# Kernel tuning notes

Measured on AMD Instinct MI355X. Metric: run time of the kernel, lower is better.

Reference implementation:

```python
import jax, jax.numpy as jnp
import numpy as np

N = 50000  # nodes
E = 800000  # edges (avg degree 16)


def gcn_agg(x, senders, receivers, n, add_self_edges):
    """jraph.GraphConvolution aggregation with symmetric normalization.
    x: [n, d] node feats already passed through update_node_fn."""
    if add_self_edges:
        idx = jnp.arange(n, dtype=senders.dtype)
        s = jnp.concatenate([senders, idx])
        r = jnp.concatenate([receivers, idx])
    else:
        s, r = senders, receivers
    ones = jnp.ones(s.shape, x.dtype)
    sdeg = jax.ops.segment_sum(ones, s, num_segments=n)
    rdeg = jax.ops.segment_sum(ones, r, num_segments=n)
    x = x * jax.lax.rsqrt(jnp.maximum(sdeg, 1.0))[:, None]
    x = jax.ops.segment_sum(x[s], r, num_segments=n)  # [E+,d] gather -> scatter-sum
    return x * jax.lax.rsqrt(jnp.maximum(rdeg, 1.0))[:, None]


def setup_inputs() -> dict:
    key = jax.random.key(0)
    ks = jax.random.split(key, 9)
    d_in, d_h, d_z, d_out = 128, 128, 64, 128

    def w(k, i, o):
        return jax.random.normal(k, (i, o), jnp.float32) / np.float32(np.sqrt(i))

    return {
        "nodes": jax.random.normal(ks[0], (N, d_in), jnp.float32),
        "senders": jax.random.randint(ks[1], (E,), 0, N, jnp.int32),
        "receivers": jax.random.randint(ks[2], (E,), 0, N, jnp.int32),
        "eps": jax.random.normal(ks[3], (N, d_z), jnp.float32),
        "W_h": w(ks[4], d_in, d_h), "b_h": jnp.zeros((d_h,), jnp.float32),
        "W_mu": w(ks[5], d_h, d_z), "b_mu": jnp.zeros((d_z,), jnp.float32),
        "W_ls": w(ks[6], d_h, d_z), "b_ls": jnp.zeros((d_z,), jnp.float32),
        "W_dh": w(ks[7], d_z, d_h), "b_dh": jnp.zeros((d_h,), jnp.float32),
        "W_do": w(ks[8], d_h, d_out), "b_do": jnp.zeros((d_out,), jnp.float32),
    }


def reference(nodes, senders, receivers, eps, W_h, b_h, W_mu, b_mu,
              W_ls, b_ls, W_dh, b_dh, W_do, b_do):
    n = nodes.shape[0]
    # encoder hidden GCN (add_self_edges=True): Linear+elu update, then agg.
    # (the first of the two identical encoder GCN calls in the source is dead
    #  code -- both read the original graph, only the 2nd result is used)
    h = jax.nn.elu(nodes @ W_h + b_h)
    h = gcn_agg(h, senders, receivers, n, True)
    # mean / log_std GCNs (add_self_edges=False)
    mean = gcn_agg(h @ W_mu + b_mu, senders, receivers, n, False)
    log_std = gcn_agg(h @ W_ls + b_ls, senders, receivers, n, False)
    # reparameterization
    z = mean + jnp.exp(log_std) * eps
    # decoder: GCN(self edges, Linear+elu) -> GCN(no self edges, Linear)
    d = jax.nn.elu(z @ W_dh + b_dh)
    d = gcn_agg(d, senders, receivers, n, True)
    out = gcn_agg(d @ W_do + b_do, senders, receivers, n, False)
    return mean, log_std, out
```

## Files before the change

kernel.cpp:

```cpp
#include <hip/hip_runtime.h>
#include <hip/hip_bf16.h>
#include <hip/hip_fp16.h>
#include <math.h>


typedef _Float16 f16x8 __attribute__((ext_vector_type(8)));
typedef _Float16 f16x4 __attribute__((ext_vector_type(4)));
typedef float    f32x4 __attribute__((ext_vector_type(4)));

union H2x4 { int4 i; __half2 h[4]; };

#define HSL 64
#define HIST_LDS_W 12544
#define NSLICE 256
#define CAP 8000

__global__ __launch_bounds__(256)
void hist8s_k(const int* __restrict__ snd, unsigned int* __restrict__ partial,
              int nE, int nW)
{
    __shared__ unsigned int sh[HIST_LDS_W];
    const int slice = blockIdx.x;
    for (int w = threadIdx.x; w < nW; w += 256) sh[w] = 0u;
    __syncthreads();
    const int per = (nE + HSL - 1) / HSL;
    const int e1 = min(nE, slice * per + per);
    for (int e = slice * per + threadIdx.x; e < e1; e += 256) {
        int v = snd[e];
        atomicAdd(&sh[v >> 2], 1u << ((v & 3) * 8));
    }
    __syncthreads();
    unsigned int* dst = partial + (size_t)slice * nW;
    for (int w = threadIdx.x; w < nW; w += 256) dst[w] = sh[w];
}

__global__ __launch_bounds__(256)
void hist8s_reduce_k(const unsigned int* __restrict__ partial,
                     float* __restrict__ dsi, float* __restrict__ dsn,
                     int n, int nW)
{
    int w = blockIdx.x * 256 + threadIdx.x;
    if (w >= nW) return;
    const unsigned int* src = partial + w;
    int c0 = 0, c1 = 0, c2 = 0, c3 = 0;
    for (int s = 0; s < HSL; ++s) {
        unsigned int v = src[(size_t)s * nW];
        c0 += v & 255u; c1 += (v >> 8) & 255u; c2 += (v >> 16) & 255u; c3 += v >> 24;
    }
    const int cc[4] = {c0, c1, c2, c3};
    const int node0 = w * 4;
#pragma unroll
    for (int u = 0; u < 4; ++u) {
        int node = node0 + u;
        if (node >= n) break;
        float fd = (float)cc[u];
        dsi[node] = rsqrtf(fd + 1.0f);
        dsn[node] = rsqrtf(fmaxf(fd, 1.0f));
    }
}

__global__ __launch_bounds__(256)
void rcount_k(const int* __restrict__ rcv, int* __restrict__ cnt, int nE, int nb)
{
    __shared__ int lc[256];
    const int s = blockIdx.x;
    if (threadIdx.x < nb) lc[threadIdx.x] = 0;
    __syncthreads();
    const int per = (nE + NSLICE - 1) / NSLICE;
    const int e1 = min(nE, (s + 1) * per);
    for (int e = s * per + threadIdx.x; e < e1; e += 256)
        atomicAdd(&lc[rcv[e] >> 8], 1);
    __syncthreads();
    if (threadIdx.x < nb) cnt[s * nb + threadIdx.x] = lc[threadIdx.x];
}

__global__ __launch_bounds__(256)
void rscan_k(const int* __restrict__ cnt, int* __restrict__ sbase,
             int* __restrict__ btot, int nb)
{
    __shared__ int sh[256];
    const int b = blockIdx.x, t = threadIdx.x;
    int v = cnt[t * nb + b];
    sh[t] = v; __syncthreads();
#pragma unroll
    for (int off = 1; off < 256; off <<= 1) {
        int u = (t >= off) ? sh[t - off] : 0;
        __syncthreads(); sh[t] += u; __syncthreads();
    }
    sbase[t * nb + b] = sh[t] - v;
    if (t == 255) btot[b] = sh[255];
}

__global__ __launch_bounds__(256)
void bscan_k(const int* __restrict__ btot, int* __restrict__ bbase,
             int* __restrict__ row_start, int nb, int n)
{
    __shared__ int sh[256];
    const int t = threadIdx.x;
    int v = (t < nb) ? btot[t] : 0;
    sh[t] = v; __syncthreads();
#pragma unroll
    for (int off = 1; off < 256; off <<= 1) {
        int u = (t >= off) ? sh[t - off] : 0;
        __syncthreads(); sh[t] += u; __syncthreads();
    }
    if (t < nb) bbase[t] = sh[t] - v;
    if (t == 255) row_start[n] = sh[255];
}

__global__ __launch_bounds__(256)
void rscatter_k(const int* __restrict__ snd, const int* __restrict__ rcv,
                const int* __restrict__ sbase, int2* __restrict__ stage,
                int nE, int nb)
{
    __shared__ int cur[256];
    const int s = blockIdx.x;
    if (threadIdx.x < nb) cur[threadIdx.x] = sbase[s * nb + threadIdx.x];
    __syncthreads();
    const int per = (nE + NSLICE - 1) / NSLICE;
    const int e1 = min(nE, (s + 1) * per);
    for (int e = s * per + threadIdx.x; e < e1; e += 256) {
        int r = rcv[e], b = r >> 8;
        int t = atomicAdd(&cur[b], 1);
        if (t < CAP) stage[(size_t)b * CAP + t] = make_int2(snd[e], r);
    }
}

__global__ __launch_bounds__(256)
void rfin_k(const int2* __restrict__ stage, const int* __restrict__ btot,
            const int* __restrict__ bbase, int* __restrict__ row_start,
            float* __restrict__ dri, float* __restrict__ drn,
            int* __restrict__ csr, int n)
{
    __shared__ int cnt[256];
    __shared__ int pos[256];
    __shared__ int lbuf[CAP];
    const int b = blockIdx.x, t = threadIdx.x;
    cnt[t] = 0;
    __syncthreads();
    const int tot = min(btot[b], CAP);
    const int2* sp = stage + (size_t)b * CAP;
    for (int i = t; i < tot; i += 256)
        atomicAdd(&cnt[sp[i].y & 255], 1);
    __syncthreads();
    const int c = cnt[t];
    pos[t] = c; __syncthreads();
#pragma unroll
    for (int off = 1; off < 256; off <<= 1) {
        int u = (t >= off) ? pos[t - off] : 0;
        __syncthreads(); pos[t] += u; __syncthreads();
    }
    const int excl = pos[t] - c;
    const int base = bbase[b];
    const int v = b * 256 + t;
    if (v < n) {
        row_start[v] = base + excl;
        float fd = (float)c;
        dri[v] = rsqrtf(fd + 1.0f);
        drn[v] = rsqrtf(fmaxf(fd, 1.0f));
    }
    cnt[t] = excl;
    __syncthreads();
    for (int i = t; i < tot; i += 256) {
        int2 p = sp[i];
        int q = atomicAdd(&cnt[p.y & 255], 1);
        lbuf[q] = p.x << 8;
    }
    __syncthreads();
    for (int i = t; i < tot; i += 256)
        csr[base + i] = lbuf[i];
}

__global__ __launch_bounds__(256)
void wprep_k(const float* __restrict__ W_h, const float* __restrict__ W_mu,
             const float* __restrict__ W_ls, const float* __restrict__ W_dh,
             const float* __restrict__ W_do,
             const float* __restrict__ b_mu, const float* __restrict__ b_ls,
             __half* __restrict__ WT_h, __half* __restrict__ WT2,
             __half* __restrict__ WT_dh, __half* __restrict__ WT_do,
             float* __restrict__ bias2)
{
    int gid = blockIdx.x * 256 + threadIdx.x;
    if (gid < 16384) {
        int m = gid >> 7, k = gid & 127;
        WT_h[gid] = __float2half(W_h[k * 128 + m]);
    } else if (gid < 32768) {
        int t = gid - 16384; int m = t >> 7, k = t & 127;
        float v = (m < 64) ? W_mu[k * 64 + m] : W_ls[k * 64 + (m - 64)];
        WT2[t] = __float2half(v);
    } else if (gid < 40960) {
        int t = gid - 32768; int m = t >> 6, k = t & 63;
        WT_dh[t] = __float2half(W_dh[k * 128 + m]);
    } else if (gid < 57344) {
        int t = gid - 40960; int m = t >> 7, k = t & 127;
        WT_do[t] = __float2half(W_do[k * 128 + m]);
    } else if (gid < 57472) {
        int c = gid - 57344;
        bias2[c] = (c < 64) ? b_mu[c] : b_ls[c - 64];
    }
}

template<int K, int ELU, typename XT>
__global__ __launch_bounds__(256)
void mgemm_k(const XT* __restrict__ X, const __half* __restrict__ WT,
             const float* __restrict__ Bias, const float* __restrict__ rowscale,
             __half* __restrict__ Y, int nrows)
{
    const int lane = threadIdx.x & 63;
    const int w    = threadIdx.x >> 6;
    const int l15  = lane & 15, l4 = lane >> 4;
    const int rowbase = blockIdx.x * 128 + w * 32;
    if (rowbase >= nrows) return;

    f32x4 acc[2][8];
#pragma unroll
    for (int mt = 0; mt < 2; ++mt)
#pragma unroll
        for (int nt = 0; nt < 8; ++nt)
#pragma unroll
            for (int q = 0; q < 4; ++q) acc[mt][nt][q] = 0.f;

    const int r0 = min(rowbase + l15,      nrows - 1);
    const int r1 = min(rowbase + 16 + l15, nrows - 1);

#pragma unroll
    for (int ks = 0; ks < K / 32; ++ks) {
        const int ko = ks * 32 + l4 * 8;
        f16x8 a0, a1;
        if constexpr (sizeof(XT) == 4) {
            const float4 p0 = *(const float4*)&X[(size_t)r0 * K + ko];
            const float4 p1 = *(const float4*)&X[(size_t)r0 * K + ko + 4];
            const float4 q0 = *(const float4*)&X[(size_t)r1 * K + ko];
            const float4 q1 = *(const float4*)&X[(size_t)r1 * K + ko + 4];
            a0[0] = (_Float16)p0.x; a0[1] = (_Float16)p0.y;
            a0[2] = (_Float16)p0.z; a0[3] = (_Float16)p0.w;
            a0[4] = (_Float16)p1.x; a0[5] = (_Float16)p1.y;
            a0[6] = (_Float16)p1.z; a0[7] = (_Float16)p1.w;
            a1[0] = (_Float16)q0.x; a1[1] = (_Float16)q0.y;
            a1[2] = (_Float16)q0.z; a1[3] = (_Float16)q0.w;
            a1[4] = (_Float16)q1.x; a1[5] = (_Float16)q1.y;
            a1[6] = (_Float16)q1.z; a1[7] = (_Float16)q1.w;
        } else {
            a0 = *(const f16x8*)&X[(size_t)r0 * K + ko];
            a1 = *(const f16x8*)&X[(size_t)r1 * K + ko];
        }
#pragma unroll
        for (int nt = 0; nt < 8; ++nt) {
            const f16x8 b = *(const f16x8*)&WT[(size_t)(nt * 16 + l15) * K + ko];
            acc[0][nt] = __builtin_amdgcn_mfma_f32_16x16x32_f16(b, a0, acc[0][nt], 0, 0, 0);
            acc[1][nt] = __builtin_amdgcn_mfma_f32_16x16x32_f16(b, a1, acc[1][nt], 0, 0, 0);
        }
    }

    const int xr0 = rowbase + l15, xr1 = rowbase + 16 + l15;
    const float rs0 = (xr0 < nrows) ? rowscale[xr0] : 0.f;
    const float rs1 = (xr1 < nrows) ? rowscale[xr1] : 0.f;
#pragma unroll
    for (int nt = 0; nt < 8; ++nt) {
        const float4 b4 = *(const float4*)&Bias[nt * 16 + l4 * 4];
        const float bb[4] = {b4.x, b4.y, b4.z, b4.w};
        f16x4 o0, o1;
#pragma unroll
        for (int i = 0; i < 4; ++i) {
            float v0 = acc[0][nt][i] + bb[i];
            float v1 = acc[1][nt][i] + bb[i];
            if (ELU) {
                v0 = (v0 > 0.f) ? v0 : expm1f(v0);
                v1 = (v1 > 0.f) ? v1 : expm1f(v1);
            }
            o0[i] = (_Float16)(v0 * rs0);
            o1[i] = (_Float16)(v1 * rs1);
        }
        if (xr0 < nrows) *(f16x4*)&Y[(size_t)xr0 * 128 + nt * 16 + l4 * 4] = o0;
        if (xr1 < nrows) *(f16x4*)&Y[(size_t)xr1 * 128 + nt * 16 + l4 * 4] = o1;
    }
}

__device__ inline void agg_core(const char* __restrict__ yb, const int* __restrict__ csr,
                                int beg, int end, int g, float2 (&acc)[4])
{
    int j = beg;
    if (j + 16 <= end) {
        int o0 = csr[j + g], o1 = csr[j + 4 + g];
        int o2 = csr[j + 8 + g], o3 = csr[j + 12 + g];
        for (; j + 32 <= end; j += 16) {
            const int p0 = csr[j + 16 + g], p1 = csr[j + 20 + g];
            const int p2 = csr[j + 24 + g], p3 = csr[j + 28 + g];
            H2x4 r0, r1, r2, r3;
            r0.i = *(const int4*)(yb + o0);
            r1.i = *(const int4*)(yb + o1);
            r2.i = *(const int4*)(yb + o2);
            r3.i = *(const int4*)(yb + o3);
#pragma unroll
            for (int k = 0; k < 4; ++k) {
                const float2 f01 = __half22float2(__hadd2(r0.h[k], r1.h[k]));
                const float2 f23 = __half22float2(__hadd2(r2.h[k], r3.h[k]));
                acc[k].x += f01.x + f23.x;
                acc[k].y += f01.y + f23.y;
            }
            o0 = p0; o1 = p1; o2 = p2; o3 = p3;
        }
        {
            H2x4 r0, r1, r2, r3;
            r0.i = *(const int4*)(yb + o0);
            r1.i = *(const int4*)(yb + o1);
            r2.i = *(const int4*)(yb + o2);
            r3.i = *(const int4*)(yb + o3);
#pragma unroll
            for (int k = 0; k < 4; ++k) {
                const float2 f01 = __half22float2(__hadd2(r0.h[k], r1.h[k]));
                const float2 f23 = __half22float2(__hadd2(r2.h[k], r3.h[k]));
                acc[k].x += f01.x + f23.x;
                acc[k].y += f01.y + f23.y;
            }
        }
        j += 16;
    }
    for (; j + 8 <= end; j += 8) {
        const int o0 = csr[j + g], o1 = csr[j + 4 + g];
        H2x4 r0, r1;
        r0.i = *(const int4*)(yb + o0);
        r1.i = *(const int4*)(yb + o1);
#pragma unroll
        for (int k = 0; k < 4; ++k) {
            const float2 f01 = __half22float2(__hadd2(r0.h[k], r1.h[k]));
            acc[k].x += f01.x;
            acc[k].y += f01.y;
        }
    }
    for (; j < end; j += 4) {
        const int e = j + g;
        const bool ok = e < end;
        const int o = csr[ok ? e : end - 1];
        H2x4 r; r.i = *(const int4*)(yb + o);
        if (ok) {
#pragma unroll
            for (int k = 0; k < 4; ++k) {
                const float2 f = __half22float2(r.h[k]);
                acc[k].x += f.x;
                acc[k].y += f.y;
            }
        }
    }
#pragma unroll
    for (int k = 0; k < 4; ++k) {
        acc[k].x += __shfl_xor(acc[k].x, 16);
        acc[k].y += __shfl_xor(acc[k].y, 16);
        acc[k].x += __shfl_xor(acc[k].x, 32);
        acc[k].y += __shfl_xor(acc[k].y, 32);
    }
}

__global__ __launch_bounds__(256)
void aggw_self_k(const __half* __restrict__ y, const int* __restrict__ row_start,
                 const int* __restrict__ csr, const float* __restrict__ rsc,
                 __half* __restrict__ out, int n)
{
    const int v    = (blockIdx.x * 256 + threadIdx.x) >> 6;
    const int lane = threadIdx.x & 63;
    if (v >= n) return;
    const int g = lane >> 4, c16 = lane & 15;
    const int beg = row_start[v], end = row_start[v + 1];
    const char* yb = (const char*)y + c16 * 16;

    float2 acc[4] = {{0.f,0.f},{0.f,0.f},{0.f,0.f},{0.f,0.f}};
    if (g == 0) {
        H2x4 r; r.i = *(const int4*)(yb + (v << 8));
#pragma unroll
        for (int k = 0; k < 4; ++k) {
            const float2 f = __half22float2(r.h[k]);
            acc[k].x += f.x; acc[k].y += f.y;
        }
    }
    agg_core(yb, csr, beg, end, g, acc);
    if (g == 0) {
        const float sc = rsc[v];
        f16x8 o;
#pragma unroll
        for (int k = 0; k < 4; ++k) {
            o[2 * k]     = (_Float16)(acc[k].x * sc);
            o[2 * k + 1] = (_Float16)(acc[k].y * sc);
        }
        *(f16x8*)&out[(size_t)v * 128 + c16 * 8] = o;
    }
}

__global__ __launch_bounds__(256)
void aggw_f32_k(const __half* __restrict__ y, const int* __restrict__ row_start,
                const int* __restrict__ csr, const float* __restrict__ rsc,
                float* __restrict__ out, int n)
{
    const int v    = (blockIdx.x * 256 + threadIdx.x) >> 6;
    const int lane = threadIdx.x & 63;
    if (v >= n) return;
    const int g = lane >> 4, c16 = lane & 15;
    const int beg = row_start[v], end = row_start[v + 1];
    const char* yb = (const char*)y + c16 * 16;

    float2 acc[4] = {{0.f,0.f},{0.f,0.f},{0.f,0.f},{0.f,0.f}};
    agg_core(yb, csr, beg, end, g, acc);
    const float sc = rsc[v];
    if (g == 0)
        *(float4*)&out[(size_t)v * 128 + c16 * 8] =
            make_float4(acc[0].x * sc, acc[0].y * sc, acc[1].x * sc, acc[1].y * sc);
    if (g == 1)
        *(float4*)&out[(size_t)v * 128 + c16 * 8 + 4] =
            make_float4(acc[2].x * sc, acc[2].y * sc, acc[3].x * sc, acc[3].y * sc);
}

__global__ __launch_bounds__(256)
void aggw_2z_k(const __half* __restrict__ y, const int* __restrict__ row_start,
               const int* __restrict__ csr, const float* __restrict__ rsc,
               const float* __restrict__ eps,
               float* __restrict__ mean, float* __restrict__ lstd,
               __half* __restrict__ z16, int n)
{
    const int v    = (blockIdx.x * 256 + threadIdx.x) >> 6;
    const int lane = threadIdx.x & 63;
    if (v >= n) return;
    const int g = lane >> 4, c16 = lane & 15;
    const int beg = row_start[v], end = row_start[v + 1];
    const char* yb = (const char*)y + c16 * 16;

    float2 acc2[4] = {{0.f,0.f},{0.f,0.f},{0.f,0.f},{0.f,0.f}};
    agg_core(yb, csr, beg, end, g, acc2);
    const float sc = rsc[v];
    float acc[8];
#pragma unroll
    for (int k = 0; k < 4; ++k) {
        acc[2 * k]     = acc2[k].x * sc;
        acc[2 * k + 1] = acc2[k].y * sc;
    }

    if (c16 < 8) {
        if (g == 0) *(float4*)&mean[(size_t)v * 64 + c16 * 8]     = make_float4(acc[0], acc[1], acc[2], acc[3]);
        if (g == 1) *(float4*)&mean[(size_t)v * 64 + c16 * 8 + 4] = make_float4(acc[4], acc[5], acc[6], acc[7]);
    } else {
        if (g == 0) *(float4*)&lstd[(size_t)v * 64 + (c16 - 8) * 8]     = make_float4(acc[0], acc[1], acc[2], acc[3]);
        if (g == 1) *(float4*)&lstd[(size_t)v * 64 + (c16 - 8) * 8 + 4] = make_float4(acc[4], acc[5], acc[6], acc[7]);
    }
    float lsv[8];
#pragma unroll
    for (int k = 0; k < 8; ++k) lsv[k] = __shfl_xor(acc[k], 8);
    if (g == 0 && c16 < 8) {
        const float4 e0 = *(const float4*)&eps[(size_t)v * 64 + c16 * 8];
        const float4 e1 = *(const float4*)&eps[(size_t)v * 64 + c16 * 8 + 4];
        const float ev[8] = {e0.x, e0.y, e0.z, e0.w, e1.x, e1.y, e1.z, e1.w};
        f16x8 o;
#pragma unroll
        for (int k = 0; k < 8; ++k) o[k] = (_Float16)(acc[k] + expf(lsv[k]) * ev[k]);
        *(f16x8*)&z16[(size_t)v * 64 + c16 * 8] = o;
    }
}

extern "C" void kernel_launch(void* const* d_in, const int* in_sizes, int n_in,
                              void* d_out, int out_size, void* d_ws, size_t ws_size,
                              hipStream_t stream)
{
    const float* nodes = (const float*)d_in[0];
    const int*   snd   = (const int*)d_in[1];
    const int*   rcv   = (const int*)d_in[2];
    const float* eps   = (const float*)d_in[3];
    const float* W_h  = (const float*)d_in[4];  const float* b_h  = (const float*)d_in[5];
    const float* W_mu = (const float*)d_in[6];  const float* b_mu = (const float*)d_in[7];
    const float* W_ls = (const float*)d_in[8];  const float* b_ls = (const float*)d_in[9];
    const float* W_dh = (const float*)d_in[10]; const float* b_dh = (const float*)d_in[11];
    const float* W_do = (const float*)d_in[12]; const float* b_do = (const float*)d_in[13];

    const int n  = in_sizes[0] / 128;
    const int nE = in_sizes[1];
    const int nW = (n + 3) >> 2;
    const int nb = (n + 255) >> 8;

    __half* bufA16 = (__half*)d_ws;
    __half* bufB16 = bufA16 + (size_t)n * 128;
    __half* bufC16 = bufB16 + (size_t)n * 128;
    float* dsi = (float*)(bufC16 + (size_t)n * 64);
    float* dri = dsi + n;
    float* dsn = dri + n;
    float* drn = dsn + n;
    int* row_start = (int*)(drn + n);
    int* csr       = row_start + n + 4;
    int* cnt       = csr + nE;
    int* sbase     = cnt + 256 * nb;
    int* btot      = sbase + 256 * nb;
    int* bbase     = btot + 256;
    __half* WT_h  = (__half*)(bbase + 256);
    __half* WT2   = WT_h + 16384;
    __half* WT_dh = WT2 + 16384;
    __half* WT_do = WT_dh + 8192;
    float*  bias2 = (float*)(WT_do + 16384);
    unsigned int* partial = (unsigned int*)bufA16;
    int2* stage = (int2*)bufB16;

    float* mean = (float*)d_out;
    float* lstd = mean + (size_t)n * 64;
    float* outp = lstd + (size_t)n * 64;

    auto cdiv = [](int a, int b) { return (a + b - 1) / b; };
    const int gG = cdiv(n, 128);
    const int gW = cdiv(n * 64, 256);

    wprep_k<<<cdiv(57472, 256), 256, 0, stream>>>(W_h, W_mu, W_ls, W_dh, W_do,
                                                  b_mu, b_ls, WT_h, WT2, WT_dh, WT_do, bias2);
    hist8s_k<<<HSL, 256, 0, stream>>>(snd, partial, nE, nW);
    hist8s_reduce_k<<<cdiv(nW, 256), 256, 0, stream>>>(partial, dsi, dsn, n, nW);
    rcount_k<<<NSLICE, 256, 0, stream>>>(rcv, cnt, nE, nb);
    rscan_k<<<nb, 256, 0, stream>>>(cnt, sbase, btot, nb);
    bscan_k<<<1, 256, 0, stream>>>(btot, bbase, row_start, nb, n);
    rscatter_k<<<NSLICE, 256, 0, stream>>>(snd, rcv, sbase, stage, nE, nb);
    rfin_k<<<nb, 256, 0, stream>>>(stage, btot, bbase, row_start, dri, drn, csr, n);

    mgemm_k<128, 1, float><<<gG, 256, 0, stream>>>(nodes, WT_h, b_h, dsi, bufA16, n);
    aggw_self_k<<<gW, 256, 0, stream>>>(bufA16, row_start, csr, dri, bufB16, n);

    mgemm_k<128, 0, __half><<<gG, 256, 0, stream>>>(bufB16, WT2, bias2, dsn, bufA16, n);
    aggw_2z_k<<<gW, 256, 0, stream>>>(bufA16, row_start, csr, drn, eps, mean, lstd, bufC16, n);

    mgemm_k<64, 1, __half><<<gG, 256, 0, stream>>>(bufC16, WT_dh, b_dh, dsi, bufA16, n);
    aggw_self_k<<<gW, 256, 0, stream>>>(bufA16, row_start, csr, dri, bufB16, n);

    mgemm_k<128, 0, __half><<<gG, 256, 0, stream>>>(bufB16, WT_do, b_do, dsn, bufA16, n);
    aggw_f32_k<<<gW, 256, 0, stream>>>(bufA16, row_start, csr, drn, outp, n);
}
```

Before: 275.3 us.

## Map one node per 16-lane group in aggregation and merge CSR count/scatter

The aggregation kernels now assign one node to each 16-lane quarter of a wavefront, so a wave handles four nodes. Each lane walks that node's full edge list serially, replacing the old scheme where four groups split the edges of one node and combined them with cross-lane shuffles. The CSR build drops its separate count, per-slice scan and scatter kernels for one kernel that reserves bucket ranges with global atomics. This cuts launches and shuffle reductions, but per-node load imbalance grows and edges land in buckets in a nondeterministic order.

Result: no change. 270.6 us (median of 2 runs) (-1.7%).

```diff
diff --git a/kernel.cpp b/kernel.cpp
--- a/kernel.cpp
+++ b/kernel.cpp
@@ -60,35 +60,29 @@
 }
 
 __global__ __launch_bounds__(256)
-void rcount_k(const int* __restrict__ rcv, int* __restrict__ cnt, int nE, int nb)
+void rscatter2_k(const int* __restrict__ snd, const int* __restrict__ rcv,
+                 int* __restrict__ gcur, int2* __restrict__ stage,
+                 int nE, int nb)
 {
     __shared__ int lc[256];
-    const int s = blockIdx.x;
-    if (threadIdx.x < nb) lc[threadIdx.x] = 0;
+    __shared__ int lbase[256];
+    const int s = blockIdx.x, t = threadIdx.x;
+    lc[t] = 0;
     __syncthreads();
     const int per = (nE + NSLICE - 1) / NSLICE;
-    const int e1 = min(nE, (s + 1) * per);
-    for (int e = s * per + threadIdx.x; e < e1; e += 256)
+    const int e0 = s * per, e1 = min(nE, e0 + per);
+    for (int e = e0 + t; e < e1; e += 256)
         atomicAdd(&lc[rcv[e] >> 8], 1);
     __syncthreads();
-    if (threadIdx.x < nb) cnt[s * nb + threadIdx.x] = lc[threadIdx.x];
-}
-
-__global__ __launch_bounds__(256)
-void rscan_k(const int* __restrict__ cnt, int* __restrict__ sbase,
-             int* __restrict__ btot, int nb)
-{
-    __shared__ int sh[256];
-    const int b = blockIdx.x, t = threadIdx.x;
-    int v = cnt[t * nb + b];
-    sh[t] = v; __syncthreads();
-#pragma unroll
-    for (int off = 1; off < 256; off <<= 1) {
-        int u = (t >= off) ? sh[t - off] : 0;
-        __syncthreads(); sh[t] += u; __syncthreads();
-    }
-    sbase[t * nb + b] = sh[t] - v;
-    if (t == 255) btot[b] = sh[255];
+    if (t < nb && lc[t] > 0) lbase[t] = atomicAdd(&gcur[t], lc[t]);
+    __syncthreads();
+    lc[t] = 0;
+    __syncthreads();
+    for (int e = e0 + t; e < e1; e += 256) {
+        int r = rcv[e], b = r >> 8;
+        int q = lbase[b] + atomicAdd(&lc[b], 1);
+        if (q < CAP) stage[(size_t)b * CAP + q] = make_int2(snd[e], r);
+    }
 }
 
 __global__ __launch_bounds__(256)
@@ -106,24 +100,6 @@
     }
     if (t < nb) bbase[t] = sh[t] - v;
     if (t == 255) row_start[n] = sh[255];
-}
-
-__global__ __launch_bounds__(256)
-void rscatter_k(const int* __restrict__ snd, const int* __restrict__ rcv,
-                const int* __restrict__ sbase, int2* __restrict__ stage,
-                int nE, int nb)
-{
-    __shared__ int cur[256];
-    const int s = blockIdx.x;
-    if (threadIdx.x < nb) cur[threadIdx.x] = sbase[s * nb + threadIdx.x];
-    __syncthreads();
-    const int per = (nE + NSLICE - 1) / NSLICE;
-    const int e1 = min(nE, (s + 1) * per);
-    for (int e = s * per + threadIdx.x; e < e1; e += 256) {
-        int r = rcv[e], b = r >> 8;
-        int t = atomicAdd(&cur[b], 1);
-        if (t < CAP) stage[(size_t)b * CAP + t] = make_int2(snd[e], r);
-    }
 }
 
 __global__ __launch_bounds__(256)
@@ -276,154 +252,106 @@
     }
 }
 
-__device__ inline void agg_core(const char* __restrict__ yb, const int* __restrict__ csr,
-                                int beg, int end, int g, float2 (&acc)[4])
+__device__ inline void agg_core2(const char* __restrict__ yb, const int* __restrict__ csr,
+                                 int beg, int end, float2 (&acc)[4])
 {
     int j = beg;
-    if (j + 16 <= end) {
-        int o0 = csr[j + g], o1 = csr[j + 4 + g];
-        int o2 = csr[j + 8 + g], o3 = csr[j + 12 + g];
-        for (; j + 32 <= end; j += 16) {
-            const int p0 = csr[j + 16 + g], p1 = csr[j + 20 + g];
-            const int p2 = csr[j + 24 + g], p3 = csr[j + 28 + g];
-            H2x4 r0, r1, r2, r3;
-            r0.i = *(const int4*)(yb + o0);
-            r1.i = *(const int4*)(yb + o1);
-            r2.i = *(const int4*)(yb + o2);
-            r3.i = *(const int4*)(yb + o3);
-#pragma unroll
-            for (int k = 0; k < 4; ++k) {
-                const float2 f01 = __half22float2(__hadd2(r0.h[k], r1.h[k]));
-                const float2 f23 = __half22float2(__hadd2(r2.h[k], r3.h[k]));
-                acc[k].x += f01.x + f23.x;
-                acc[k].y += f01.y + f23.y;
-            }
-            o0 = p0; o1 = p1; o2 = p2; o3 = p3;
-        }
-        {
-            H2x4 r0, r1, r2, r3;
-            r0.i = *(const int4*)(yb + o0);
-            r1.i = *(const int4*)(yb + o1);
-            r2.i = *(const int4*)(yb + o2);
-            r3.i = *(const int4*)(yb + o3);
-#pragma unroll
-            for (int k = 0; k < 4; ++k) {
-                const float2 f01 = __half22float2(__hadd2(r0.h[k], r1.h[k]));
-                const float2 f23 = __half22float2(__hadd2(r2.h[k], r3.h[k]));
-                acc[k].x += f01.x + f23.x;
-                acc[k].y += f01.y + f23.y;
-            }
-        }
-        j += 16;
-    }
-    for (; j + 8 <= end; j += 8) {
-        const int o0 = csr[j + g], o1 = csr[j + 4 + g];
-        H2x4 r0, r1;
+    for (; j + 4 <= end; j += 4) {
+        const int o0 = csr[j], o1 = csr[j + 1], o2 = csr[j + 2], o3 = csr[j + 3];
+        H2x4 r0, r1, r2, r3;
         r0.i = *(const int4*)(yb + o0);
         r1.i = *(const int4*)(yb + o1);
+        r2.i = *(const int4*)(yb + o2);
+        r3.i = *(const int4*)(yb + o3);
 #pragma unroll
         for (int k = 0; k < 4; ++k) {
             const float2 f01 = __half22float2(__hadd2(r0.h[k], r1.h[k]));
-            acc[k].x += f01.x;
-            acc[k].y += f01.y;
+            const float2 f23 = __half22float2(__hadd2(r2.h[k], r3.h[k]));
+            acc[k].x += f01.x + f23.x;
+            acc[k].y += f01.y + f23.y;
         }
     }
-    for (; j < end; j += 4) {
-        const int e = j + g;
-        const bool ok = e < end;
-        const int o = csr[ok ? e : end - 1];
+    for (; j < end; ++j) {
+        const int o = csr[j];
         H2x4 r; r.i = *(const int4*)(yb + o);
-        if (ok) {
-#pragma unroll
-            for (int k = 0; k < 4; ++k) {
-                const float2 f = __half22float2(r.h[k]);
-                acc[k].x += f.x;
-                acc[k].y += f.y;
-            }
+#pragma unroll
+        for (int k = 0; k < 4; ++k) {
+            const float2 f = __half22float2(r.h[k]);
+            acc[k].x += f.x;
+            acc[k].y += f.y;
         }
     }
-#pragma unroll
-    for (int k = 0; k < 4; ++k) {
-        acc[k].x += __shfl_xor(acc[k].x, 16);
-        acc[k].y += __shfl_xor(acc[k].y, 16);
-        acc[k].x += __shfl_xor(acc[k].x, 32);
-        acc[k].y += __shfl_xor(acc[k].y, 32);
-    }
-}
-
-__global__ __launch_bounds__(256)
-void aggw_self_k(const __half* __restrict__ y, const int* __restrict__ row_start,
+}
+
+__global__ __launch_bounds__(256)
+void aggg_self_k(const __half* __restrict__ y, const int* __restrict__ row_start,
                  const int* __restrict__ csr, const float* __restrict__ rsc,
                  __half* __restrict__ out, int n)
 {
-    const int v    = (blockIdx.x * 256 + threadIdx.x) >> 6;
-    const int lane = threadIdx.x & 63;
+    const int wid = (blockIdx.x * 256 + threadIdx.x) >> 6;
+    const int g   = (threadIdx.x >> 4) & 3;
+    const int l16 = threadIdx.x & 15;
+    const int v   = wid * 4 + g;
     if (v >= n) return;
-    const int g = lane >> 4, c16 = lane & 15;
     const int beg = row_start[v], end = row_start[v + 1];
-    const char* yb = (const char*)y + c16 * 16;
-
-    float2 acc[4] = {{0.f,0.f},{0.f,0.f},{0.f,0.f},{0.f,0.f}};
-    if (g == 0) {
+    const char* yb = (const char*)y + l16 * 16;
+
+    float2 acc[4];
+    {
         H2x4 r; r.i = *(const int4*)(yb + (v << 8));
 #pragma unroll
-        for (int k = 0; k < 4; ++k) {
-            const float2 f = __half22float2(r.h[k]);
-            acc[k].x += f.x; acc[k].y += f.y;
-        }
-    }
-    agg_core(yb, csr, beg, end, g, acc);
-    if (g == 0) {
-        const float sc = rsc[v];
-        f16x8 o;
-#pragma unroll
-        for (int k = 0; k < 4; ++k) {
-            o[2 * k]     = (_Float16)(acc[k].x * sc);
-            o[2 * k + 1] = (_Float16)(acc[k].y * sc);
-        }
-        *(f16x8*)&out[(size_t)v * 128 + c16 * 8] = o;
-    }
-}
-
-__global__ __launch_bounds__(256)
-void aggw_f32_k(const __half* __restrict__ y, const int* __restrict__ row_start,
+        for (int k = 0; k < 4; ++k) acc[k] = __half22float2(r.h[k]);
+    }
+    agg_core2(yb, csr, beg, end, acc);
+    const float sc = rsc[v];
+    f16x8 o;
+#pragma unroll
+    for (int k = 0; k < 4; ++k) {
+        o[2 * k]     = (_Float16)(acc[k].x * sc);
+        o[2 * k + 1] = (_Float16)(acc[k].y * sc);
+    }
+    *(f16x8*)&out[(size_t)v * 128 + l16 * 8] = o;
+}
+
+__global__ __launch_bounds__(256)
+void aggg_f32_k(const __half* __restrict__ y, const int* __restrict__ row_start,
                 const int* __restrict__ csr, const float* __restrict__ rsc,
                 float* __restrict__ out, int n)
 {
-    const int v    = (blockIdx.x * 256 + threadIdx.x) >> 6;
-    const int lane = threadIdx.x & 63;
+    const int wid = (blockIdx.x * 256 + threadIdx.x) >> 6;
+    const int g   = (threadIdx.x >> 4) & 3;
+    const int l16 = threadIdx.x & 15;
+    const int v   = wid * 4 + g;
     if (v >= n) return;
-    const int g = lane >> 4, c16 = lane & 15;
     const int beg = row_start[v], end = row_start[v + 1];
-    const char* yb = (const char*)y + c16 * 16;
+    const char* yb = (const char*)y + l16 * 16;
 
     float2 acc[4] = {{0.f,0.f},{0.f,0.f},{0.f,0.f},{0.f,0.f}};
-    agg_core(yb, csr, beg, end, g, acc);
+    agg_core2(yb, csr, beg, end, acc);
     const float sc = rsc[v];
-    if (g == 0)
-        *(float4*)&out[(size_t)v * 128 + c16 * 8] =
-            make_float4(acc[0].x * sc, acc[0].y * sc, acc[1].x * sc, acc[1].y * sc);
-    if (g == 1)
-        *(float4*)&out[(size_t)v * 128 + c16 * 8 + 4] =
-            make_float4(acc[2].x * sc, acc[2].y * sc, acc[3].x * sc, acc[3].y * sc);
-}
-
-__global__ __launch_bounds__(256)
-void aggw_2z_k(const __half* __restrict__ y, const int* __restrict__ row_start,
+    *(float4*)&out[(size_t)v * 128 + l16 * 8] =
+        make_float4(acc[0].x * sc, acc[0].y * sc, acc[1].x * sc, acc[1].y * sc);
+    *(float4*)&out[(size_t)v * 128 + l16 * 8 + 4] =
+        make_float4(acc[2].x * sc, acc[2].y * sc, acc[3].x * sc, acc[3].y * sc);
+}
+
+__global__ __launch_bounds__(256)
+void aggg_2z_k(const __half* __restrict__ y, const int* __restrict__ row_start,
                const int* __restrict__ csr, const float* __restrict__ rsc,
                const float* __restrict__ eps,
                float* __restrict__ mean, float* __restrict__ lstd,
                __half* __restrict__ z16, int n)
 {
-    const int v    = (blockIdx.x * 256 + threadIdx.x) >> 6;
-    const int lane = threadIdx.x & 63;
+    const int wid = (blockIdx.x * 256 + threadIdx.x) >> 6;
+    const int g   = (threadIdx.x >> 4) & 3;
+    const int l16 = threadIdx.x & 15;
+    const int v   = wid * 4 + g;
     if (v >= n) return;
-    const int g = lane >> 4, c16 = lane & 15;
     const int beg = row_start[v], end = row_start[v + 1];
-    const char* yb = (const char*)y + c16 * 16;
+    const char* yb = (const char*)y + l16 * 16;
 
     float2 acc2[4] = {{0.f,0.f},{0.f,0.f},{0.f,0.f},{0.f,0.f}};
-    agg_core(yb, csr, beg, end, g, acc2);
+    agg_core2(yb, csr, beg, end, acc2);
     const float sc = rsc[v];
     float acc[8];
 #pragma unroll
@@ -432,24 +360,24 @@
         acc[2 * k + 1] = acc2[k].y * sc;
     }
 
-    if (c16 < 8) {
-        if (g == 0) *(float4*)&mean[(size_t)v * 64 + c16 * 8]     = make_float4(acc[0], acc[1], acc[2], acc[3]);
-        if (g == 1) *(float4*)&mean[(size_t)v * 64 + c16 * 8 + 4] = make_float4(acc[4], acc[5], acc[6], acc[7]);
+    if (l16 < 8) {
+        *(float4*)&mean[(size_t)v * 64 + l16 * 8]     = make_float4(acc[0], acc[1], acc[2], acc[3]);
+        *(float4*)&mean[(size_t)v * 64 + l16 * 8 + 4] = make_float4(acc[4], acc[5], acc[6], acc[7]);
     } else {
-        if (g == 0) *(float4*)&lstd[(size_t)v * 64 + (c16 - 8) * 8]     = make_float4(acc[0], acc[1], acc[2], acc[3]);
-        if (g == 1) *(float4*)&lstd[(size_t)v * 64 + (c16 - 8) * 8 + 4] = make_float4(acc[4], acc[5], acc[6], acc[7]);
+        *(float4*)&lstd[(size_t)v * 64 + (l16 - 8) * 8]     = make_float4(acc[0], acc[1], acc[2], acc[3]);
+        *(float4*)&lstd[(size_t)v * 64 + (l16 - 8) * 8 + 4] = make_float4(acc[4], acc[5], acc[6], acc[7]);
     }
     float lsv[8];
 #pragma unroll
     for (int k = 0; k < 8; ++k) lsv[k] = __shfl_xor(acc[k], 8);
-    if (g == 0 && c16 < 8) {
-        const float4 e0 = *(const float4*)&eps[(size_t)v * 64 + c16 * 8];
-        const float4 e1 = *(const float4*)&eps[(size_t)v * 64 + c16 * 8 + 4];
+    if (l16 < 8) {
+        const float4 e0 = *(const float4*)&eps[(size_t)v * 64 + l16 * 8];
+        const float4 e1 = *(const float4*)&eps[(size_t)v * 64 + l16 * 8 + 4];
         const float ev[8] = {e0.x, e0.y, e0.z, e0.w, e1.x, e1.y, e1.z, e1.w};
         f16x8 o;
 #pragma unroll
         for (int k = 0; k < 8; ++k) o[k] = (_Float16)(acc[k] + expf(lsv[k]) * ev[k]);
-        *(f16x8*)&z16[(size_t)v * 64 + c16 * 8] = o;
+        *(f16x8*)&z16[(size_t)v * 64 + l16 * 8] = o;
     }
 }
 
@@ -481,10 +409,8 @@
     float* drn = dsn + n;
     int* row_start = (int*)(drn + n);
     int* csr       = row_start + n + 4;
-    int* cnt       = csr + nE;
-    int* sbase     = cnt + 256 * nb;
-    int* btot      = sbase + 256 * nb;
-    int* bbase     = btot + 256;
+    int* gcur      = csr + nE;
+    int* bbase     = gcur + 256;
     __half* WT_h  = (__half*)(bbase + 256);
     __half* WT2   = WT_h + 16384;
     __half* WT_dh = WT2 + 16384;
@@ -498,28 +424,27 @@
     float* outp = lstd + (size_t)n * 64;
 
     auto cdiv = [](int a, int b) { return (a + b - 1) / b; };
-    const int gG = cdiv(n, 128);
-    const int gW = cdiv(n * 64, 256);
+    const int gG  = cdiv(n, 128);
+    const int gW4 = cdiv(n * 16, 256);
 
     wprep_k<<<cdiv(57472, 256), 256, 0, stream>>>(W_h, W_mu, W_ls, W_dh, W_do,
                                                   b_mu, b_ls, WT_h, WT2, WT_dh, WT_do, bias2);
     hist8s_k<<<HSL, 256, 0, stream>>>(snd, partial, nE, nW);
     hist8s_reduce_k<<<cdiv(nW, 256), 256, 0, stream>>>(partial, dsi, dsn, n, nW);
-    rcount_k<<<NSLICE, 256, 0, stream>>>(rcv, cnt, nE, nb);
-    rscan_k<<<nb, 256, 0, stream>>>(cnt, sbase, btot, nb);
-    bscan_k<<<1, 256, 0, stream>>>(btot, bbase, row_start, nb, n);
-    rscatter_k<<<NSLICE, 256, 0, stream>>>(snd, rcv, sbase, stage, nE, nb);
-    rfin_k<<<nb, 256, 0, stream>>>(stage, btot, bbase, row_start, dri, drn, csr, n);
+    hipMemsetAsync(gcur, 0, nb * sizeof(int), stream);
+    rscatter2_k<<<NSLICE, 256, 0, stream>>>(snd, rcv, gcur, stage, nE, nb);
+    bscan_k<<<1, 256, 0, stream>>>(gcur, bbase, row_start, nb, n);
+    rfin_k<<<nb, 256, 0, stream>>>(stage, gcur, bbase, row_start, dri, drn, csr, n);
 
     mgemm_k<128, 1, float><<<gG, 256, 0, stream>>>(nodes, WT_h, b_h, dsi, bufA16, n);
-    aggw_self_k<<<gW, 256, 0, stream>>>(bufA16, row_start, csr, dri, bufB16, n);
+    aggg_self_k<<<gW4, 256, 0, stream>>>(bufA16, row_start, csr, dri, bufB16, n);
 
     mgemm_k<128, 0, __half><<<gG, 256, 0, stream>>>(bufB16, WT2, bias2, dsn, bufA16, n);
-    aggw_2z_k<<<gW, 256, 0, stream>>>(bufA16, row_start, csr, drn, eps, mean, lstd, bufC16, n);
+    aggg_2z_k<<<gW4, 256, 0, stream>>>(bufA16, row_start, csr, drn, eps, mean, lstd, bufC16, n);
 
     mgemm_k<64, 1, __half><<<gG, 256, 0, stream>>>(bufC16, WT_dh, b_dh, dsi, bufA16, n);
-    aggw_self_k<<<gW, 256, 0, stream>>>(bufA16, row_start, csr, dri, bufB16, n);
+    aggg_self_k<<<gW4, 256, 0, stream>>>(bufA16, row_start, csr, dri, bufB16, n);
 
     mgemm_k<128, 0, __half><<<gG, 256, 0, stream>>>(bufB16, WT_do, b_do, dsn, bufA16, n);
-    aggw_f32_k<<<gW, 256, 0, stream>>>(bufA16, row_start, csr, drn, outp, n);
-}
+    aggg_f32_k<<<gW4, 256, 0, stream>>>(bufA16, row_start, csr, drn, outp, n);
+}
```
